# Performance work log

Measured on AMD Instinct MI355X. Metric: run time of the kernel, lower is better.

## Reference

```python
import jax, jax.numpy as jnp
import numpy as np

D = 1024
H = 16
DH = D // H  # 64

def setup_inputs() -> dict:
    key = jax.random.key(0)
    ks = jax.random.split(key, 9)
    B, L = 2, 2048
    s = 1.0 / np.sqrt(D)
    inp = {
        'x':  jax.random.normal(ks[0], (B, L, D), dtype=jnp.float32),
        'Wq': jax.random.uniform(ks[1], (D, D), jnp.float32, -s, s),
        'bq': jnp.zeros((D,), jnp.float32),
        'Wk': jax.random.uniform(ks[2], (D, D), jnp.float32, -s, s),
        'bk': jnp.zeros((D,), jnp.float32),
        'Wv': jax.random.uniform(ks[3], (D, D), jnp.float32, -s, s),
        'bv': jnp.zeros((D,), jnp.float32),
        'Wo': jax.random.uniform(ks[4], (D, D), jnp.float32, -s, s),
        'bo': jnp.zeros((D,), jnp.float32),
    }
    return inp

def reference(x, Wq, bq, Wk, bk, Wv, bv, Wo, bo):
    B, L, _ = x.shape
    # projections (torch Linear: x @ W.T + b; here weights stored as [D_in, D_out])
    q = (x @ Wq + bq).reshape(B, L, H, DH).transpose(0, 2, 1, 3)  # [B,H,L,DH]
    k = (x @ Wk + bk).reshape(B, L, H, DH).transpose(0, 2, 1, 3)
    v = (x @ Wv + bv).reshape(B, L, H, DH).transpose(0, 2, 1, 3)
    scores = jnp.einsum('bhqd,bhkd->bhqk', q, k) / jnp.sqrt(jnp.float32(DH))
    attn = jax.nn.softmax(scores, axis=-1)  # dropout p=0 / eval -> identity
    out = jnp.einsum('bhqk,bhkd->bhqd', attn, v)
    out = out.transpose(0, 2, 1, 3).reshape(B, L, D)
    return out @ Wo + bo
```

## Files before the change

kernel.cpp:

```cpp
#include <hip/hip_runtime.h>
#include <stdint.h>

typedef __attribute__((ext_vector_type(8)))  __bf16 bf16x8;
typedef __attribute__((ext_vector_type(4)))  __bf16 bf16x4;
typedef __attribute__((ext_vector_type(4)))  float  f32x4;
typedef __attribute__((ext_vector_type(16))) float  f32x16;
typedef __attribute__((ext_vector_type(4)))  int    i32x4;

#define DEV static __device__ __forceinline__

DEV float fast_exp2(float x) {
#if __has_builtin(__builtin_amdgcn_exp2f)
  return __builtin_amdgcn_exp2f(x);
#else
  return exp2f(x);
#endif
}

DEV uint32_t pack_bf2(float a, float b) {
  __bf16 x = (__bf16)a, y = (__bf16)b;
  uint16_t xu = __builtin_bit_cast(uint16_t, x);
  uint16_t yu = __builtin_bit_cast(uint16_t, y);
  return (uint32_t)xu | ((uint32_t)yu << 16);
}

DEV void gload_lds16(const void* g, void* l) {
  __builtin_amdgcn_global_load_lds(
      (const __attribute__((address_space(1))) void*)(uintptr_t)(g),
      (__attribute__((address_space(3))) void*)(uint32_t)(uintptr_t)(l),
      16, 0, 0);
}

#define SM_SCALE 0.18033688f

__global__ void k_prep(const float* __restrict__ x,  __bf16* __restrict__ xb,
                       const float* __restrict__ Wq, const float* __restrict__ Wk,
                       const float* __restrict__ Wv, const float* __restrict__ Wo,
                       __bf16* __restrict__ wtq, __bf16* __restrict__ wot) {
  const int z = blockIdx.z;
  if (z < 4) {
    const float* W  = (z == 0) ? Wq : (z == 1) ? Wk : (z == 2) ? Wv : Wo;
    __bf16*      Wt = (z == 3) ? wot : (wtq + (size_t)z * 1024 * 1024);
    __shared__ __bf16 T[64][66];
    int t = threadIdx.x;
    int r = t >> 2;
    int cq = (t & 3) << 4;
    {
      int gk = blockIdx.y * 64 + r;
      int gn0 = blockIdx.x * 64 + cq;
      const float* src = W + (size_t)gk * 1024 + gn0;
#pragma unroll
      for (int j = 0; j < 16; j += 4) {
        f32x4 v = *(const f32x4*)(src + j);
#pragma unroll
        for (int jj = 0; jj < 4; ++jj) T[r][cq + j + jj] = (__bf16)v[jj];
      }
    }
    __syncthreads();
    {
      int gn = blockIdx.x * 64 + r;
      int gk0 = blockIdx.y * 64 + cq;
      __bf16* dst = Wt + (size_t)gn * 1024 + gk0;
      bf16x8 o0, o1;
#pragma unroll
      for (int j = 0; j < 8; ++j) { o0[j] = T[cq + j][r]; o1[j] = T[cq + 8 + j][r]; }
      *(bf16x8*)dst = o0;
      *(bf16x8*)(dst + 8) = o1;
    }
  } else {
    int lb = (z - 4) * 256 + blockIdx.y * 16 + blockIdx.x;
    int i = (lb * 256 + (int)threadIdx.x) * 4;
    if (i < 4096 * 1024) {
      f32x4 v = *(const f32x4*)(x + i);
      bf16x4 o;
      o[0] = (__bf16)v[0]; o[1] = (__bf16)v[1];
      o[2] = (__bf16)v[2]; o[3] = (__bf16)v[3];
      *(bf16x4*)(xb + i) = o;
    }
  }
}

__global__ void k_vt(const __bf16* __restrict__ qkv, __bf16* __restrict__ Vt) {
  __shared__ __bf16 T[64][66];
  int lt = blockIdx.x, bh = blockIdx.y;
  int b = bh >> 4, h = bh & 15;
  int t = threadIdx.x;
  int r = t >> 2, cq = (t & 3) << 4;
  {
    const __bf16* src = qkv + (size_t)(b * 2048 + lt * 64 + r) * 3072 + 2048 + h * 64 + cq;
    bf16x8 v0 = *(const bf16x8*)src;
    bf16x8 v1 = *(const bf16x8*)(src + 8);
#pragma unroll
    for (int j = 0; j < 8; ++j) { T[r][cq + j] = v0[j]; T[r][cq + 8 + j] = v1[j]; }
  }
  __syncthreads();
  {
    __bf16* dst = Vt + (size_t)(bh * 64 + r) * 2048 + lt * 64 + cq;
    bf16x8 o0, o1;
#pragma unroll
    for (int j = 0; j < 8; ++j) { o0[j] = T[cq + j][r]; o1[j] = T[cq + 8 + j][r]; }
    *(bf16x8*)dst = o0;
    *(bf16x8*)(dst + 8) = o1;
  }
}

__global__ void k_gemm0(const __bf16* __restrict__ A, const __bf16* __restrict__ Bt,
                        __bf16* __restrict__ Cout, int M, int N, int K,
                        const float* __restrict__ b0, const float* __restrict__ b1,
                        const float* __restrict__ b2) {
  __shared__ __align__(16) __bf16 As[128 * 64];
  __shared__ __align__(16) __bf16 Bs[128 * 64];
  const int t = threadIdx.x, wid = t >> 6, lane = t & 63;
  const int bm = blockIdx.y, bn = blockIdx.x;
  const int wm = wid >> 1, wn = wid & 1;
  const int l15 = lane & 15, l4 = lane >> 4;
  const int rr = lane >> 3, cc = lane & 7;
  f32x4 acc[4][4] = {};
  const int nk = K >> 6;
  for (int kt = 0; kt < nk; ++kt) {
    __syncthreads();
#pragma unroll
    for (int j = 0; j < 4; ++j) {
      int row = wid * 32 + j * 8 + rr;
      int csrc = (cc ^ (row & 7)) * 8;
      gload_lds16(A + (size_t)(bm * 128 + row) * K + kt * 64 + csrc,
                  (char*)As + (wid * 32 + j * 8) * 128);
      gload_lds16(Bt + (size_t)(bn * 128 + row) * K + kt * 64 + csrc,
                  (char*)Bs + (wid * 32 + j * 8) * 128);
    }
    __syncthreads();
#pragma unroll
    for (int kk = 0; kk < 2; ++kk) {
      bf16x8 a[4], b[4];
#pragma unroll
      for (int ms = 0; ms < 4; ++ms) {
        int row = wm * 64 + ms * 16 + l15;
        a[ms] = *(const bf16x8*)((char*)As + row * 128 + (((kk * 4 + l4) ^ (row & 7)) * 16));
      }
#pragma unroll
      for (int ns = 0; ns < 4; ++ns) {
        int row = wn * 64 + ns * 16 + l15;
        b[ns] = *(const bf16x8*)((char*)Bs + row * 128 + (((kk * 4 + l4) ^ (row & 7)) * 16));
      }
#pragma unroll
      for (int ms = 0; ms < 4; ++ms)
#pragma unroll
        for (int ns = 0; ns < 4; ++ns)
          acc[ms][ns] = __builtin_amdgcn_mfma_f32_16x16x32_bf16(a[ms], b[ns], acc[ms][ns], 0, 0, 0);
    }
  }
#pragma unroll
  for (int ms = 0; ms < 4; ++ms) {
#pragma unroll
    for (int ns = 0; ns < 4; ++ns) {
      int n = bn * 128 + wn * 64 + ns * 16 + l15;
      const float* bp = (n < 1024) ? b0 : ((n < 2048) ? b1 : b2);
      float bias = bp[n & 1023];
#pragma unroll
      for (int i = 0; i < 4; ++i) {
        int m = bm * 128 + wm * 64 + ms * 16 + l4 * 4 + i;
        float v = acc[ms][ns][i] + bias;
        if (n < 1024) v *= SM_SCALE;
        Cout[(size_t)m * N + n] = (__bf16)v;
      }
    }
  }
}

__global__ void k_gemm64(const __bf16* __restrict__ A, const __bf16* __restrict__ Bt,
                         float* __restrict__ Cout, int M, int N, int K,
                         const float* __restrict__ b0) {
  __shared__ __align__(16) __bf16 As[64 * 64];
  __shared__ __align__(16) __bf16 Bs[64 * 64];
  const int t = threadIdx.x, wid = t >> 6, lane = t & 63;
  const int bm = blockIdx.y, bn = blockIdx.x;
  const int wm = wid >> 1, wn = wid & 1;
  const int l15 = lane & 15, l4 = lane >> 4;
  const int rr = lane >> 3, cc = lane & 7;
  f32x4 acc[2][2] = {};
  const int nk = K >> 6;
  for (int kt = 0; kt < nk; ++kt) {
    __syncthreads();
#pragma unroll
    for (int j = 0; j < 2; ++j) {
      int row = wid * 16 + j * 8 + rr;
      int csrc = (cc ^ (row & 7)) * 8;
      gload_lds16(A + (size_t)(bm * 64 + row) * K + kt * 64 + csrc,
                  (char*)As + (wid * 16 + j * 8) * 128);
      gload_lds16(Bt + (size_t)(bn * 64 + row) * K + kt * 64 + csrc,
                  (char*)Bs + (wid * 16 + j * 8) * 128);
    }
    __syncthreads();
#pragma unroll
    for (int kk = 0; kk < 2; ++kk) {
      bf16x8 a[2], b[2];
#pragma unroll
      for (int ms = 0; ms < 2; ++ms) {
        int row = wm * 32 + ms * 16 + l15;
        a[ms] = *(const bf16x8*)((char*)As + row * 128 + (((kk * 4 + l4) ^ (row & 7)) * 16));
      }
#pragma unroll
      for (int ns = 0; ns < 2; ++ns) {
        int row = wn * 32 + ns * 16 + l15;
        b[ns] = *(const bf16x8*)((char*)Bs + row * 128 + (((kk * 4 + l4) ^ (row & 7)) * 16));
      }
#pragma unroll
      for (int ms = 0; ms < 2; ++ms)
#pragma unroll
        for (int ns = 0; ns < 2; ++ns)
          acc[ms][ns] = __builtin_amdgcn_mfma_f32_16x16x32_bf16(a[ms], b[ns], acc[ms][ns], 0, 0, 0);
    }
  }
#pragma unroll
  for (int ms = 0; ms < 2; ++ms) {
#pragma unroll
    for (int ns = 0; ns < 2; ++ns) {
      int n = bn * 64 + wn * 32 + ns * 16 + l15;
      float bias = b0[n];
#pragma unroll
      for (int i = 0; i < 4; ++i) {
        int m = bm * 64 + wm * 32 + ms * 16 + l4 * 4 + i;
        Cout[(size_t)m * N + n] = acc[ms][ns][i] + bias;
      }
    }
  }
}

__global__ void __launch_bounds__(256, 6)
k_attn(const __bf16* __restrict__ qkv, const __bf16* __restrict__ Vt,
       __bf16* __restrict__ Aout) {
  __shared__ __align__(16) char smem[32768];
  const int t = threadIdx.x, w = t >> 6, lane = t & 63;
  const int qsub = w & 1, half = w >> 1;
  const int l31 = lane & 31, hi = lane >> 5;
  const int f = blockIdx.x;
  const int qt = (f >> 3) & 31;
  const int bh = (f & 7) + 8 * (f >> 8);
  const int b = bh >> 4, h = bh & 15;
  const int kv0 = half * 1024;

  const __bf16* Kg = qkv + (size_t)(b * 2048) * 3072 + 1024 + h * 64;
  const __bf16* Vg = Vt + (size_t)(bh * 64) * 2048;

  bf16x8 aq[4];
  {
    int qrow = b * 2048 + qt * 64 + qsub * 32 + l31;
    const __bf16* qp = qkv + (size_t)qrow * 3072 + h * 64 + hi * 8;
#pragma unroll
    for (int d = 0; d < 4; ++d) aq[d] = *(const bf16x8*)(qp + d * 16);
  }

  f32x16 o[2] = {};
  float lsum = 0.f;

  char* Kbase = smem + half * 16384;

  auto STAGE = [&](int bi, int kt) {
    char* Kl = Kbase + bi * 8192;
    char* Vl = Kl + 4096;
    const __bf16* kg = Kg + (size_t)(kv0 + kt * 32) * 3072;
    const __bf16* vg = Vg + (kv0 + kt * 32);
#pragma unroll
    for (int j = 0; j < 2; ++j) {
      int g = qsub * 2 + j;
      gload_lds16(kg + (size_t)l31 * 3072 + (g * 2 + hi) * 8, Kl + g * 1024);
      gload_lds16(vg + (size_t)((g & 1) * 32 + l31) * 2048 + ((g >> 1) * 2 + hi) * 8,
                  Vl + g * 1024);
    }
  };

  STAGE(0, 0);
  __syncthreads();

  int cur = 0;
  for (int kt = 0; kt < 32; ++kt) {
    if (kt < 31) STAGE(cur ^ 1, kt + 1);
    const char* Kv = Kbase + cur * 8192 + lane * 16;
    const char* Vv = Kv + 4096;

    f32x16 s;
    s = 0.f;
    __builtin_amdgcn_s_setprio(1);
#pragma unroll
    for (int d = 0; d < 4; ++d) {
      bf16x8 kf = *(const bf16x8*)(Kv + d * 1024);
      s = __builtin_amdgcn_mfma_f32_32x32x16_bf16(kf, aq[d], s, 0, 0, 0);
    }
    __builtin_amdgcn_s_setprio(0);

#pragma unroll
    for (int r = 0; r < 16; ++r) s[r] = fast_exp2(s[r]);

    {
      float u[8];
#pragma unroll
      for (int c = 0; c < 8; ++c) u[c] = s[2 * c] + s[2 * c + 1];
#pragma unroll
      for (int st = 4; st > 0; st >>= 1)
#pragma unroll
        for (int c = 0; c < st; ++c) u[c] += u[c + st];
      lsum += u[0];
    }

    uint32_t W[8];
#pragma unroll
    for (int c = 0; c < 8; ++c) W[c] = pack_bf2(s[2 * c], s[2 * c + 1]);

    bf16x8 pa[2];
#pragma unroll
    for (int kstep = 0; kstep < 2; ++kstep) {
      const int base = 4 * kstep;
      uint32_t w0 = W[base + 0], w1 = W[base + 1];
      uint32_t w2 = W[base + 2], w3 = W[base + 3];
      uint32_t x0 = __shfl_xor((int)w0, 32);
      uint32_t x1 = __shfl_xor((int)w1, 32);
      uint32_t x2 = __shfl_xor((int)w2, 32);
      uint32_t x3 = __shfl_xor((int)w3, 32);
      i32x4 pw;
      pw[0] = (int)(hi ? x2 : w0);
      pw[1] = (int)(hi ? x3 : w1);
      pw[2] = (int)(hi ? w2 : x0);
      pw[3] = (int)(hi ? w3 : x1);
      pa[kstep] = __builtin_bit_cast(bf16x8, pw);
    }

    __builtin_amdgcn_s_setprio(1);
#pragma unroll
    for (int kstep = 0; kstep < 2; ++kstep)
#pragma unroll
      for (int db = 0; db < 2; ++db) {
        bf16x8 vf = *(const bf16x8*)(Vv + (kstep * 2 + db) * 1024);
        o[db] = __builtin_amdgcn_mfma_f32_32x32x16_bf16(pa[kstep], vf, o[db], 0, 0, 0);
      }
    __builtin_amdgcn_s_setprio(0);

    __syncthreads();
    cur ^= 1;
  }

  lsum += __shfl_xor(lsum, 32);

  float* oLDS = (float*)smem;
  float* sLDS = (float*)(smem + 16384);
  if (half == 1) {
    float* ob = oLDS + qsub * 2048;
#pragma unroll
    for (int db = 0; db < 2; ++db)
#pragma unroll
      for (int r = 0; r < 16; ++r)
        ob[(db * 16 + r) * 64 + lane] = o[db][r];
    sLDS[qsub * 64 + lane] = lsum;
  }
  __syncthreads();
  if (half == 0) {
    const float* ob = oLDS + qsub * 2048;
#pragma unroll
    for (int db = 0; db < 2; ++db)
#pragma unroll
      for (int r = 0; r < 16; ++r)
        o[db][r] += ob[(db * 16 + r) * 64 + lane];
    lsum += sLDS[qsub * 64 + lane];

#pragma unroll
    for (int r = 0; r < 16; ++r) {
      int rowq = (r & 3) + 8 * (r >> 2) + 4 * hi;
      float inv = 1.0f / __shfl(lsum, rowq);
      int qg = b * 2048 + qt * 64 + qsub * 32 + rowq;
#pragma unroll
      for (int db = 0; db < 2; ++db) {
        int col = h * 64 + db * 32 + l31;
        Aout[(size_t)qg * 1024 + col] = (__bf16)(o[db][r] * inv);
      }
    }
  }
}

extern "C" void kernel_launch(void* const* d_in, const int* in_sizes, int n_in,
                              void* d_out, int out_size, void* d_ws, size_t ws_size,
                              hipStream_t stream) {
  const float* x  = (const float*)d_in[0];
  const float* Wq = (const float*)d_in[1];
  const float* bq = (const float*)d_in[2];
  const float* Wk = (const float*)d_in[3];
  const float* bk = (const float*)d_in[4];
  const float* Wv = (const float*)d_in[5];
  const float* bv = (const float*)d_in[6];
  const float* Wo = (const float*)d_in[7];
  const float* bo = (const float*)d_in[8];
  float* out = (float*)d_out;

  char* ws = (char*)d_ws;
  __bf16* xb   = (__bf16*)(ws);
  __bf16* wtq  = (__bf16*)(ws + (8ull  << 20));
  __bf16* wot  = (__bf16*)(ws + (14ull << 20));
  __bf16* qkv  = (__bf16*)(ws + (16ull << 20));
  __bf16* vt   = (__bf16*)(ws + (40ull << 20));
  __bf16* aout = (__bf16*)(ws + (48ull << 20));

  k_prep<<<dim3(16, 16, 20), 256, 0, stream>>>(x, xb, Wq, Wk, Wv, Wo, wtq, wot);

  k_gemm0<<<dim3(24, 32), 256, 0, stream>>>(xb, wtq, qkv, 4096, 3072, 1024, bq, bk, bv);

  k_vt<<<dim3(32, 32), 256, 0, stream>>>(qkv, vt);

  k_attn<<<dim3(1024), 256, 0, stream>>>(qkv, vt, aout);

  k_gemm64<<<dim3(16, 64), 256, 0, stream>>>(aout, wot, out, 4096, 1024, 1024, bo);
}
```

Baseline: 130.3 us.

## Pre-swizzle K/V into fragment layout and load directly to registers in attention

The transpose kernel now also writes K, and both K and V go into a per-tile layout that matches the MFMA fragments. Each lane can then load its operands straight from global memory with contiguous 16-byte reads. The attention kernel drops its LDS double-buffering and per-iteration __syncthreads, and instead prefetches into registers with a two-stage ping-pong. This removes the LDS staging and barrier costs, but adds register pressure (launch bounds lowered to 3 blocks per SM) and an extra copy of K. The workspace is also reused by aliasing aout onto xb.

```diff
diff --git a/kernel.cpp b/kernel.cpp
--- a/kernel.cpp
+++ b/kernel.cpp
@@ -80,13 +80,27 @@
   }
 }
 
-__global__ void k_vt(const __bf16* __restrict__ qkv, __bf16* __restrict__ Vt) {
-  __shared__ __bf16 T[64][66];
-  int lt = blockIdx.x, bh = blockIdx.y;
+__global__ void k_vt(const __bf16* __restrict__ qkv, __bf16* __restrict__ kvf) {
+  int lt = blockIdx.x, bh = blockIdx.y, z = blockIdx.z;
   int b = bh >> 4, h = bh & 15;
   int t = threadIdx.x;
-  int r = t >> 2, cq = (t & 3) << 4;
+  int lane = t & 63, slot = t >> 6;
+  int l31 = lane & 31, hi = lane >> 5;
+
+  if (z == 1) {
+#pragma unroll
+    for (int tt = 0; tt < 2; ++tt) {
+      const __bf16* src = qkv + (size_t)(b * 2048 + lt * 64 + tt * 32 + l31) * 3072
+                          + 1024 + h * 64 + slot * 16 + hi * 8;
+      __bf16* dst = kvf + (size_t)(bh * 64 + lt * 2 + tt) * 4096 + slot * 512 + lane * 8;
+      *(bf16x8*)dst = *(const bf16x8*)src;
+    }
+    return;
+  }
+
+  __shared__ __bf16 T[64][66];
   {
+    int r = t >> 2, cq = (t & 3) << 4;
     const __bf16* src = qkv + (size_t)(b * 2048 + lt * 64 + r) * 3072 + 2048 + h * 64 + cq;
     bf16x8 v0 = *(const bf16x8*)src;
     bf16x8 v1 = *(const bf16x8*)(src + 8);
@@ -94,13 +108,14 @@
     for (int j = 0; j < 8; ++j) { T[r][cq + j] = v0[j]; T[r][cq + 8 + j] = v1[j]; }
   }
   __syncthreads();
-  {
-    __bf16* dst = Vt + (size_t)(bh * 64 + r) * 2048 + lt * 64 + cq;
-    bf16x8 o0, o1;
-#pragma unroll
-    for (int j = 0; j < 8; ++j) { o0[j] = T[cq + j][r]; o1[j] = T[cq + 8 + j][r]; }
-    *(bf16x8*)dst = o0;
-    *(bf16x8*)(dst + 8) = o1;
+#pragma unroll
+  for (int tt = 0; tt < 2; ++tt) {
+    bf16x8 val;
+#pragma unroll
+    for (int j = 0; j < 8; ++j)
+      val[j] = T[tt * 32 + ((slot >> 1) * 2 + hi) * 8 + j][(slot & 1) * 32 + l31];
+    __bf16* dst = kvf + (size_t)(bh * 64 + lt * 2 + tt) * 4096 + 2048 + slot * 512 + lane * 8;
+    *(bf16x8*)dst = val;
   }
 }
 
@@ -226,10 +241,10 @@
   }
 }
 
-__global__ void __launch_bounds__(256, 6)
-k_attn(const __bf16* __restrict__ qkv, const __bf16* __restrict__ Vt,
+__global__ void __launch_bounds__(256, 3)
+k_attn(const __bf16* __restrict__ qkv, const __bf16* __restrict__ kvf,
        __bf16* __restrict__ Aout) {
-  __shared__ __align__(16) char smem[32768];
+  __shared__ __align__(16) char smem[16896];
   const int t = threadIdx.x, w = t >> 6, lane = t & 63;
   const int qsub = w & 1, half = w >> 1;
   const int l31 = lane & 31, hi = lane >> 5;
@@ -237,10 +252,8 @@
   const int qt = (f >> 3) & 31;
   const int bh = (f & 7) + 8 * (f >> 8);
   const int b = bh >> 4, h = bh & 15;
-  const int kv0 = half * 1024;
-
-  const __bf16* Kg = qkv + (size_t)(b * 2048) * 3072 + 1024 + h * 64;
-  const __bf16* Vg = Vt + (size_t)(bh * 64) * 2048;
+
+  const char* kvbase = (const char*)kvf + (size_t)(bh * 64 + half * 32) * 8192 + lane * 16;
 
   bf16x8 aq[4];
   {
@@ -253,54 +266,36 @@
   f32x16 o[2] = {};
   float lsum = 0.f;
 
-  char* Kbase = smem + half * 16384;
-
-  auto STAGE = [&](int bi, int kt) {
-    char* Kl = Kbase + bi * 8192;
-    char* Vl = Kl + 4096;
-    const __bf16* kg = Kg + (size_t)(kv0 + kt * 32) * 3072;
-    const __bf16* vg = Vg + (kv0 + kt * 32);
-#pragma unroll
-    for (int j = 0; j < 2; ++j) {
-      int g = qsub * 2 + j;
-      gload_lds16(kg + (size_t)l31 * 3072 + (g * 2 + hi) * 8, Kl + g * 1024);
-      gload_lds16(vg + (size_t)((g & 1) * 32 + l31) * 2048 + ((g >> 1) * 2 + hi) * 8,
-                  Vl + g * 1024);
-    }
+  bf16x8 kA[4], vA[4], kB[4], vB[4];
+
+  auto LOAD = [&](bf16x8* kf, bf16x8* vf, int tl) {
+    const char* p = kvbase + (size_t)tl * 8192;
+#pragma unroll
+    for (int i = 0; i < 4; ++i) kf[i] = *(const bf16x8*)(p + i * 1024);
+#pragma unroll
+    for (int i = 0; i < 4; ++i) vf[i] = *(const bf16x8*)(p + 4096 + i * 1024);
   };
 
-  STAGE(0, 0);
-  __syncthreads();
-
-  int cur = 0;
-  for (int kt = 0; kt < 32; ++kt) {
-    if (kt < 31) STAGE(cur ^ 1, kt + 1);
-    const char* Kv = Kbase + cur * 8192 + lane * 16;
-    const char* Vv = Kv + 4096;
-
+  auto BODY = [&](const bf16x8* kf, const bf16x8* vf) {
     f32x16 s;
     s = 0.f;
     __builtin_amdgcn_s_setprio(1);
 #pragma unroll
-    for (int d = 0; d < 4; ++d) {
-      bf16x8 kf = *(const bf16x8*)(Kv + d * 1024);
-      s = __builtin_amdgcn_mfma_f32_32x32x16_bf16(kf, aq[d], s, 0, 0, 0);
-    }
+    for (int d = 0; d < 4; ++d)
+      s = __builtin_amdgcn_mfma_f32_32x32x16_bf16(kf[d], aq[d], s, 0, 0, 0);
     __builtin_amdgcn_s_setprio(0);
 
 #pragma unroll
     for (int r = 0; r < 16; ++r) s[r] = fast_exp2(s[r]);
 
-    {
-      float u[8];
-#pragma unroll
-      for (int c = 0; c < 8; ++c) u[c] = s[2 * c] + s[2 * c + 1];
-#pragma unroll
-      for (int st = 4; st > 0; st >>= 1)
-#pragma unroll
-        for (int c = 0; c < st; ++c) u[c] += u[c + st];
-      lsum += u[0];
-    }
+    float u[8];
+#pragma unroll
+    for (int c = 0; c < 8; ++c) u[c] = s[2 * c] + s[2 * c + 1];
+#pragma unroll
+    for (int st = 4; st > 0; st >>= 1)
+#pragma unroll
+      for (int c = 0; c < st; ++c) u[c] += u[c + st];
+    lsum += u[0];
 
     uint32_t W[8];
 #pragma unroll
@@ -328,14 +323,17 @@
 #pragma unroll
     for (int kstep = 0; kstep < 2; ++kstep)
 #pragma unroll
-      for (int db = 0; db < 2; ++db) {
-        bf16x8 vf = *(const bf16x8*)(Vv + (kstep * 2 + db) * 1024);
-        o[db] = __builtin_amdgcn_mfma_f32_32x32x16_bf16(pa[kstep], vf, o[db], 0, 0, 0);
-      }
+      for (int db = 0; db < 2; ++db)
+        o[db] = __builtin_amdgcn_mfma_f32_32x32x16_bf16(pa[kstep], vf[kstep * 2 + db], o[db], 0, 0, 0);
     __builtin_amdgcn_s_setprio(0);
-
-    __syncthreads();
-    cur ^= 1;
+  };
+
+  LOAD(kA, vA, 0);
+  for (int tl = 0; tl < 32; tl += 2) {
+    LOAD(kB, vB, tl + 1);
+    BODY(kA, vA);
+    if (tl + 2 < 32) LOAD(kA, vA, tl + 2);
+    BODY(kB, vB);
   }
 
   lsum += __shfl_xor(lsum, 32);
@@ -391,19 +389,19 @@
 
   char* ws = (char*)d_ws;
   __bf16* xb   = (__bf16*)(ws);
+  __bf16* aout = (__bf16*)(ws);
   __bf16* wtq  = (__bf16*)(ws + (8ull  << 20));
   __bf16* wot  = (__bf16*)(ws + (14ull << 20));
   __bf16* qkv  = (__bf16*)(ws + (16ull << 20));
-  __bf16* vt   = (__bf16*)(ws + (40ull << 20));
-  __bf16* aout = (__bf16*)(ws + (48ull << 20));
+  __bf16* kvf  = (__bf16*)(ws + (40ull << 20));
 
   k_prep<<<dim3(16, 16, 20), 256, 0, stream>>>(x, xb, Wq, Wk, Wv, Wo, wtq, wot);
 
   k_gemm0<<<dim3(24, 32), 256, 0, stream>>>(xb, wtq, qkv, 4096, 3072, 1024, bq, bk, bv);
 
-  k_vt<<<dim3(32, 32), 256, 0, stream>>>(qkv, vt);
-
-  k_attn<<<dim3(1024), 256, 0, stream>>>(qkv, vt, aout);
+  k_vt<<<dim3(32, 32, 2), 256, 0, stream>>>(qkv, kvf);
+
+  k_attn<<<dim3(1024), 256, 0, stream>>>(qkv, kvf, aout);
 
   k_gemm64<<<dim3(16, 64), 256, 0, stream>>>(aout, wot, out, 4096, 1024, 1024, bo);
 }
```

After: 114.6 us. -12.0%, faster.
